# Kernel optimization log

Hardware: AMD Instinct MI355X
Metric: run time of the kernel (lower is better)

Reference implementation:

```python
import jax, jax.numpy as jnp
import numpy as np

N_NODES = 50000
N_EDGES = 800000
IN_CH = 256
OUT_CH = 128
HID = 2 * OUT_CH  # 256
LN_EPS = 1e-5


def _add_self_loops(edge_index, n):
    loop = jnp.arange(n, dtype=edge_index.dtype)
    src = jnp.concatenate([edge_index[0], loop])
    dst = jnp.concatenate([edge_index[1], loop])
    return src, dst


def _gcn_norm(src, dst, n):
    # PyG GCNConv norm: deg over source index, symmetric normalization
    ones = jnp.ones(src.shape[0], dtype=jnp.float32)
    deg = jax.ops.segment_sum(ones, src, num_segments=n)
    dinv = jnp.where(deg > 0, deg ** -0.5, 0.0)
    return dinv[src] * dinv[dst]  # [E+N]


def _gcn_conv(x, src, dst, norm, w, b, gamma=None, beta=None):
    h = x @ w                              # [N, out]
    msgs = norm[:, None] * h[src]          # gather + scale, [E+N, out]
    out = jax.ops.segment_sum(msgs, dst, num_segments=x.shape[0])
    if gamma is not None:
        out = gamma * out + beta           # FiLM modulation (per-feature)
    return out + b


def _layernorm(x):
    mu = jnp.mean(x, axis=-1, keepdims=True)
    var = jnp.var(x, axis=-1, keepdims=True)
    return (x - mu) * jax.lax.rsqrt(var + LN_EPS)


def setup_inputs() -> dict:
    key = jax.random.key(0)
    ks = jax.random.split(key, 20)

    def g(k, shape, scale=0.05):
        return jax.random.normal(k, shape, dtype=jnp.float32) * scale

    x = jax.random.normal(ks[0], (N_NODES, IN_CH), dtype=jnp.float32)
    edge_index = jax.random.randint(ks[1], (2, N_EDGES), 0, N_NODES, dtype=jnp.int64)
    return {
        "x": x,
        "edge_index": edge_index,
        "conv1_w": g(ks[2], (IN_CH, HID)),
        "conv1_b": g(ks[3], (HID,)),
        "conv2_w": g(ks[4], (HID, OUT_CH)),
        "conv2_b": g(ks[5], (OUT_CH,)),
        "sig_conv_w": g(ks[6], (IN_CH, HID)),
        "sig_conv_b": g(ks[7], (HID,)),
        "fc1_w": g(ks[8], (HID, HID)),
        "fc1_b": g(ks[9], (HID,)),
        "fc2_w": g(ks[10], (HID, HID)),
        "fc2_b": g(ks[11], (HID,)),
        "fc3_w": g(ks[12], (OUT_CH, HID)),
        "fc3_b": g(ks[13], (OUT_CH,)),
        "fc4_w": g(ks[14], (OUT_CH, HID)),
        "fc4_b": g(ks[15], (OUT_CH,)),
    }


def reference(x, edge_index, conv1_w, conv1_b, conv2_w, conv2_b,
              sig_conv_w, sig_conv_b, fc1_w, fc1_b, fc2_w, fc2_b,
              fc3_w, fc3_b, fc4_w, fc4_b):
    n = x.shape[0]
    src, dst = _add_self_loops(edge_index, n)
    norm = _gcn_norm(src, dst, n)

    # --- GraphSignature (use_gcn_sig=True) ---
    s = jax.nn.relu(_gcn_conv(x, src, dst, norm, sig_conv_w, sig_conv_b))
    s = s.sum(0)  # [HID]
    gamma1 = jnp.tanh(s @ fc1_w.T + fc1_b)  # [HID]
    beta1 = jnp.tanh(s @ fc2_w.T + fc2_b)   # [HID]
    gamma2 = jnp.tanh(s @ fc3_w.T + fc3_b)  # [OUT]
    beta2 = jnp.tanh(s @ fc4_w.T + fc4_b)   # [OUT]

    # inner_loop=True: signature outputs are detached
    gamma1, beta1, gamma2, beta2 = map(jax.lax.stop_gradient,
                                       (gamma1, beta1, gamma2, beta2))

    # --- Encoder (GAE) ---
    h = jax.nn.relu(_gcn_conv(x, src, dst, norm, conv1_w, conv1_b,
                              gamma=gamma1, beta=beta1))
    h = _layernorm(h)
    out = _gcn_conv(h, src, dst, norm, conv2_w, conv2_b,
                    gamma=gamma2, beta=beta2)
    out = _layernorm(out)
    return out
```

## Files before the change

### kernel.cpp

```cpp
#include <hip/hip_runtime.h>

typedef _Float16 f16;
typedef f16 f16x8 __attribute__((ext_vector_type(8)));
typedef float f32x4 __attribute__((ext_vector_type(4)));
typedef unsigned short u16;
typedef unsigned int u32;

#define IN_CH  256
#define HID    256
#define OUT_CH 128
#define LN_EPS 1e-5f
#define NSLOT  32
#define NR     8
#define NC     32
#define RS     6272
#define HT     512


__global__ __launch_bounds__(HT) void k_hist(const int* __restrict__ ei, int nE, int nN,
                                             int* __restrict__ hP,
                                             const float* __restrict__ x, f16* __restrict__ xh,
                                             int nelem, int nCast,
                                             const float* __restrict__ sigw,
                                             const float* __restrict__ c1w,
                                             const float* __restrict__ c2w,
                                             f16* __restrict__ Wt1, f16* __restrict__ Wt2) {
    int bid = blockIdx.x;
    if (bid < NR * NC) {
        __shared__ int h[RS];
        int r = bid & (NR - 1), c = bid >> 3;
        int rsz = (nN + NR - 1) / NR;
        int r0 = r * rsz;
        int sz = nN - r0; if (sz > rsz) sz = rsz;
        for (int i = threadIdx.x; i < sz; i += HT) h[i] = 0;
        __syncthreads();
        int nT = nE + nN;
        int chunk = (nT + NC - 1) / NC;
        int e0 = c * chunk, e1 = e0 + chunk; if (e1 > nT) e1 = nT;
        for (int eb = e0 + (int)threadIdx.x; eb < e1; eb += HT * 4) {
            int ss[4], dd[4];
            #pragma unroll
            for (int u = 0; u < 4; u++) {
                int e = eb + u * HT;
                ss[u] = -1; dd[u] = -1;
                if (e < e1) {
                    if (e < nE) { ss[u] = ei[e]; dd[u] = ei[nE + e]; }
                    else { ss[u] = e - nE; dd[u] = e - nE; }
                }
            }
            #pragma unroll
            for (int u = 0; u < 4; u++) {
                if ((unsigned)(ss[u] - r0) < (unsigned)sz) atomicAdd(&h[ss[u] - r0], 1);
                if ((unsigned)(dd[u] - r0) < (unsigned)sz) atomicAdd(&h[dd[u] - r0], 0x10000);
            }
        }
        __syncthreads();
        for (int i = threadIdx.x; i < sz; i += HT) hP[(size_t)c * nN + r0 + i] = h[i];
    } else if (bid < NR * NC + nCast) {
        int i = (bid - NR * NC) * 4096 + threadIdx.x * 8;
        if (i >= nelem) return;
        float4 a = *(const float4*)(x + i);
        float4 b = *(const float4*)(x + i + 4);
        f16x8 o = { (f16)a.x, (f16)a.y, (f16)a.z, (f16)a.w,
                    (f16)b.x, (f16)b.y, (f16)b.z, (f16)b.w };
        *(f16x8*)(xh + i) = o;
    } else {
        int i = (bid - NR * NC - nCast) * HT + threadIdx.x;
        if (i < 16384) {
            int ct = i >> 9;
            int rem = i & 511;
            int kx = rem >> 6;
            int lane = rem & 63;
            int q = lane >> 4, l = lane & 15;
            int n = (ct & 15) * 16 + l;
            int k0 = kx * 32 + q * 8;
            const float* src = (ct < 16) ? sigw : c1w;
            f16x8 o;
            #pragma unroll
            for (int j = 0; j < 8; j++) o[j] = (f16)src[(size_t)(k0 + j) * 256 + n];
            *(f16x8*)(Wt1 + (size_t)i * 8) = o;
        } else if (i < 20480) {
            int h2 = i - 16384;
            int ct = h2 >> 9;
            int rem = h2 & 511;
            int kx = rem >> 6;
            int lane = rem & 63;
            int q = lane >> 4, l = lane & 15;
            int n = ct * 16 + l;
            int k0 = kx * 32 + q * 8;
            f16x8 o;
            #pragma unroll
            for (int j = 0; j < 8; j++) o[j] = (f16)c2w[(size_t)(k0 + j) * 128 + n];
            *(f16x8*)(Wt2 + (size_t)h2 * 8) = o;
        }
    }
}


__global__ __launch_bounds__(256) void k_alloc(const int* __restrict__ hP,
                                               int* __restrict__ rowstart,
                                               int* __restrict__ chunkbase,
                                               int* __restrict__ cnt_tot,
                                               float* __restrict__ dinv,
                                               int* __restrict__ ctr, int nN) {
    int i = blockIdx.x * 256 + threadIdx.x;
    int lane = threadIdx.x & 63;
    int cnt = 0, dg = 0;
    if (i < nN) {
        for (int c = 0; c < NC; c++) {
            unsigned pk = (unsigned)hP[(size_t)c * nN + i];
            cnt += (int)(pk >> 16);
            dg  += (int)(pk & 0xffffu);
        }
    }
    int p = cnt;
    #pragma unroll
    for (int off = 1; off < 64; off <<= 1) {
        int v = __shfl_up(p, off, 64);
        if (lane >= off) p += v;
    }
    int tot = __shfl(p, 63, 64);
    int base = 0;
    if (lane == 0) base = atomicAdd(ctr, tot);
    base = __shfl(base, 0, 64);
    if (i < nN) {
        int nb = base + p - cnt;
        rowstart[i] = nb;
        cnt_tot[i] = cnt;
        dinv[i] = rsqrtf((float)dg);
        int run = nb;
        for (int c = 0; c < NC; c++) {
            chunkbase[(size_t)c * nN + i] = run;
            run += (int)((unsigned)hP[(size_t)c * nN + i] >> 16);
        }
    }
}


__global__ __launch_bounds__(HT) void k_fill(const int* __restrict__ ei, int nE, int nN,
                                             const int* __restrict__ chunkbase,
                                             u16* __restrict__ src_sorted) {
    __shared__ int pos_[RS];
    int r = blockIdx.x & (NR - 1), c = blockIdx.x >> 3;
    int rsz = (nN + NR - 1) / NR;
    int r0 = r * rsz;
    int sz = nN - r0; if (sz > rsz) sz = rsz;
    for (int i = threadIdx.x; i < sz; i += HT)
        pos_[i] = chunkbase[(size_t)c * nN + r0 + i];
    __syncthreads();
    int nT = nE + nN;
    int chunk = (nT + NC - 1) / NC;
    int e0 = c * chunk, e1 = e0 + chunk; if (e1 > nT) e1 = nT;
    for (int eb = e0 + (int)threadIdx.x; eb < e1; eb += HT * 4) {
        int ss[4], dd[4];
        #pragma unroll
        for (int u = 0; u < 4; u++) {
            int e = eb + u * HT;
            ss[u] = -1; dd[u] = -1;
            if (e < e1) {
                if (e < nE) { ss[u] = ei[e]; dd[u] = ei[nE + e]; }
                else { ss[u] = e - nE; dd[u] = e - nE; }
            }
        }
        #pragma unroll
        for (int u = 0; u < 4; u++) {
            int l = dd[u] - r0;
            if ((unsigned)l < (unsigned)sz) {
                int pos = atomicAdd(&pos_[l], 1);
                src_sorted[pos] = (u16)ss[u];
            }
        }
    }
}


__global__ __launch_bounds__(256) void k_aggX(const f16* __restrict__ xh,
                                              const int* __restrict__ rowstart,
                                              const int* __restrict__ counts,
                                              const u16* __restrict__ srcs,
                                              const float* __restrict__ dinv,
                                              f16* __restrict__ AX, int nN) {
    int wv = threadIdx.x >> 6;
    int lane = threadIdx.x & 63;
    int node = blockIdx.x * 4 + wv;
    if (node >= nN) return;
    int h = lane >> 5, sub = lane & 31;
    int beg = rowstart[node];
    int cnt = counts[node];
    float acc0[8] = {}, acc1[8] = {};
    for (int base = 0; base < cnt; base += 64) {
        int el = base + lane;
        int sv = 0; float dv = 0.f;
        if (el < cnt) { sv = srcs[beg + el]; dv = dinv[sv]; }
        int rem = cnt - base; if (rem > 64) rem = 64;
        int e = 0;
        for (; e + 16 <= rem; e += 16) {
            int s_[8]; float n_[8];
            #pragma unroll
            for (int u = 0; u < 8; u++) {
                int ii = e + u * 2 + h;
                s_[u] = __shfl(sv, ii, 64);
                n_[u] = __shfl(dv, ii, 64);
            }
            f16x8 v_[8];
            #pragma unroll
            for (int u = 0; u < 8; u++)
                v_[u] = *(const f16x8*)(xh + (size_t)s_[u] * 256 + sub * 8);
            #pragma unroll
            for (int u = 0; u < 8; u++)
                #pragma unroll
                for (int j = 0; j < 8; j++) {
                    float* a = (u & 1) ? acc1 : acc0;
                    a[j] = fmaf(n_[u], (float)v_[u][j], a[j]);
                }
        }
        for (; e < rem; e += 8) {
            int i0 = e + h, i1 = e + 2 + h, i2 = e + 4 + h, i3 = e + 6 + h;
            int sa = __shfl(sv, i0, 64), sb = __shfl(sv, i1, 64);
            int sc = __shfl(sv, i2, 64), sd = __shfl(sv, i3, 64);
            float na = __shfl(dv, i0, 64), nb = __shfl(dv, i1, 64);
            float nc = __shfl(dv, i2, 64), nd = __shfl(dv, i3, 64);
            if (i0 >= rem) na = 0.f;
            if (i1 >= rem) nb = 0.f;
            if (i2 >= rem) nc = 0.f;
            if (i3 >= rem) nd = 0.f;
            f16x8 va = *(const f16x8*)(xh + (size_t)sa * 256 + sub * 8);
            f16x8 vb = *(const f16x8*)(xh + (size_t)sb * 256 + sub * 8);
            f16x8 vc = *(const f16x8*)(xh + (size_t)sc * 256 + sub * 8);
            f16x8 vd = *(const f16x8*)(xh + (size_t)sd * 256 + sub * 8);
            #pragma unroll
            for (int j = 0; j < 8; j++) {
                acc0[j] = fmaf(na, (float)va[j], acc0[j]);
                acc1[j] = fmaf(nb, (float)vb[j], acc1[j]);
                acc0[j] = fmaf(nc, (float)vc[j], acc0[j]);
                acc1[j] = fmaf(nd, (float)vd[j], acc1[j]);
            }
        }
    }
    float dn = dinv[node];
    #pragma unroll
    for (int j = 0; j < 8; j++) {
        acc0[j] += acc1[j];
        acc0[j] += __shfl_xor(acc0[j], 32, 64);
    }
    if (lane < 32) {
        f16x8 o;
        #pragma unroll
        for (int j = 0; j < 8; j++) o[j] = (f16)(acc0[j] * dn);
        *(f16x8*)(AX + (size_t)node * 256 + sub * 8) = o;
    }
}


__global__ __launch_bounds__(256) void k_gemm_sig(const f16* __restrict__ AX,
                                                  const f16* __restrict__ Wt,
                                                  const float* __restrict__ sigb,
                                                  float* __restrict__ sig_part, int M) {
    __shared__ f16 axs[32][256];
    __shared__ f16 tile[32][264];
    f16* axl = &axs[0][0];
    int t = threadIdx.x;
    int w = t >> 6, lane = t & 63, quad = lane >> 4, l16 = lane & 15;
    int m0 = blockIdx.x * 32;
    {
        int tr = t >> 5;
        int c  = t & 31;
        #pragma unroll
        for (int p = 0; p < 4; p++) {
            int row = p * 8 + tr;
            int grow = m0 + row; if (grow >= M) grow = M - 1;
            *(f16x8*)(axl + row * 256 + ((c ^ tr) << 3)) =
                *(const f16x8*)(AX + (size_t)grow * 256 + c * 8);
        }
    }
    __syncthreads();
    int cb = w * 64;
    int sw = l16 & 7;
    f32x4 acc[2][4] = {};
    for (int kx = 0; kx < 8; kx++) {
        int c0 = (kx * 4 + quad) ^ sw;
        f16x8 a[2];
        a[0] = *(const f16x8*)(axl + l16 * 256 + (c0 << 3));
        a[1] = *(const f16x8*)(axl + (16 + l16) * 256 + (c0 << 3));
        #pragma unroll
        for (int ns = 0; ns < 4; ns++) {
            int ct = w * 4 + ns;
            f16x8 b = *(const f16x8*)(Wt + ((size_t)((ct * 8 + kx) * 64 + lane) << 3));
            acc[0][ns] = __builtin_amdgcn_mfma_f32_16x16x32_f16(a[0], b, acc[0][ns], 0, 0, 0);
            acc[1][ns] = __builtin_amdgcn_mfma_f32_16x16x32_f16(a[1], b, acc[1][ns], 0, 0, 0);
        }
    }
    #pragma unroll
    for (int ms = 0; ms < 2; ms++)
        #pragma unroll
        for (int ns = 0; ns < 4; ns++)
            #pragma unroll
            for (int r = 0; r < 4; r++) {
                int mr = ms * 16 + quad * 4 + r;
                int c = cb + ns * 16 + l16;
                float v = fmaxf(acc[ms][ns][r] + sigb[c], 0.f);
                if (m0 + mr >= M) v = 0.f;
                tile[mr][c] = (f16)v;
            }
    __syncthreads();
    float s = 0.f;
    #pragma unroll 8
    for (int r = 0; r < 32; r++) s += (float)tile[r][t];
    atomicAdd(&sig_part[(blockIdx.x & (NSLOT - 1)) * 256 + t], s);
}


__global__ __launch_bounds__(256) void k_fc(const float* __restrict__ sig_part,
                                            const float* __restrict__ f1w, const float* __restrict__ f1b,
                                            const float* __restrict__ f2w, const float* __restrict__ f2b,
                                            const float* __restrict__ f3w, const float* __restrict__ f3b,
                                            const float* __restrict__ f4w, const float* __restrict__ f4b,
                                            const float* __restrict__ c1b, const float* __restrict__ c2b,
                                            float* __restrict__ g1, float* __restrict__ bc1,
                                            float* __restrict__ g2, float* __restrict__ bc2) {
    __shared__ float ss[256];
    int t = threadIdx.x;
    float s = 0.f;
    for (int k = 0; k < NSLOT; k++) s += sig_part[k * 256 + t];
    ss[t] = s;
    __syncthreads();
    int wv = t >> 6, lane = t & 63;
    float s0 = ss[lane], s1 = ss[lane + 64], s2v = ss[lane + 128], s3 = ss[lane + 192];
    #pragma unroll
    for (int rr = 0; rr < 16; rr++) {
        int row = blockIdx.x * 64 + wv * 16 + rr;
        const float* w; const float* bb; const float* ex; float* dst; int r;
        if (row < 256)      { w = f1w; bb = f1b; dst = g1;  ex = 0;   r = row; }
        else if (row < 512) { w = f2w; bb = f2b; dst = bc1; ex = c1b; r = row - 256; }
        else if (row < 640) { w = f3w; bb = f3b; dst = g2;  ex = 0;   r = row - 512; }
        else                { w = f4w; bb = f4b; dst = bc2; ex = c2b; r = row - 640; }
        const float* wr = w + (size_t)r * 256;
        float a = wr[lane] * s0;
        a = fmaf(wr[lane + 64], s1, a);
        a = fmaf(wr[lane + 128], s2v, a);
        a = fmaf(wr[lane + 192], s3, a);
        #pragma unroll
        for (int off = 1; off < 64; off <<= 1) a += __shfl_xor(a, off, 64);
        if (lane == 0) dst[r] = tanhf(a + bb[r]) + (ex ? ex[r] : 0.f);
    }
}


__global__ __launch_bounds__(256) void k_c1f(const f16* __restrict__ AX,
                                             const f16* __restrict__ Wt,
                                             const f16* __restrict__ Wt2,
                                             const float* __restrict__ g1,
                                             const float* __restrict__ bc1,
                                             const float* __restrict__ dinv,
                                             f16* __restrict__ HW, int M) {
    __shared__ f16 axs[32][256];
    __shared__ f16 ht[32][264];
    __shared__ float ps[32][5], ps2[32][5];
    __shared__ float mu_[32], rr_[32], sdinv[32];
    f16* axl = &axs[0][0];
    int t = threadIdx.x;
    int w = t >> 6, lane = t & 63, quad = lane >> 4, l16 = lane & 15;
    int m0 = blockIdx.x * 32;
    int cb = w * 64;
    {
        int tr = t >> 5;
        int c  = t & 31;
        #pragma unroll
        for (int p = 0; p < 4; p++) {
            int row = p * 8 + tr;
            int grow = m0 + row; if (grow >= M) grow = M - 1;
            *(f16x8*)(axl + row * 256 + ((c ^ tr) << 3)) =
                *(const f16x8*)(AX + (size_t)grow * 256 + c * 8);
        }
    }
    __syncthreads();
    int sw = l16 & 7;
    f32x4 acc[2][4] = {};
    for (int kx = 0; kx < 8; kx++) {
        int c0 = (kx * 4 + quad) ^ sw;
        f16x8 a[2];
        a[0] = *(const f16x8*)(axl + l16 * 256 + (c0 << 3));
        a[1] = *(const f16x8*)(axl + (16 + l16) * 256 + (c0 << 3));
        #pragma unroll
        for (int ns = 0; ns < 4; ns++) {
            int ct = w * 4 + ns;
            f16x8 b = *(const f16x8*)(Wt + ((size_t)((ct * 8 + kx) * 64 + lane) << 3));
            acc[0][ns] = __builtin_amdgcn_mfma_f32_16x16x32_f16(a[0], b, acc[0][ns], 0, 0, 0);
            acc[1][ns] = __builtin_amdgcn_mfma_f32_16x16x32_f16(a[1], b, acc[1][ns], 0, 0, 0);
        }
    }

    float rs[2][4] = {{0.f,0.f,0.f,0.f},{0.f,0.f,0.f,0.f}};
    float rs2[2][4] = {{0.f,0.f,0.f,0.f},{0.f,0.f,0.f,0.f}};
    #pragma unroll
    for (int ns = 0; ns < 4; ns++) {
        int c = cb + ns * 16 + l16;
        float gv = g1[c], bv = bc1[c];
        #pragma unroll
        for (int ms = 0; ms < 2; ms++)
            #pragma unroll
            for (int r = 0; r < 4; r++) {
                float v = fmaxf(fmaf(gv, acc[ms][ns][r], bv), 0.f);
                acc[ms][ns][r] = v;
                rs[ms][r] += v;
                rs2[ms][r] = fmaf(v, v, rs2[ms][r]);
            }
    }
    #pragma unroll
    for (int off = 1; off < 16; off <<= 1)
        #pragma unroll
        for (int ms = 0; ms < 2; ms++)
            #pragma unroll
            for (int r = 0; r < 4; r++) {
                rs[ms][r]  += __shfl_xor(rs[ms][r], off, 64);
                rs2[ms][r] += __shfl_xor(rs2[ms][r], off, 64);
            }
    if (l16 == 0) {
        #pragma unroll
        for (int ms = 0; ms < 2; ms++)
            #pragma unroll
            for (int r = 0; r < 4; r++) {
                int mr = ms * 16 + quad * 4 + r;
                ps[mr][w] = rs[ms][r];
                ps2[mr][w] = rs2[ms][r];
            }
    }
    __syncthreads();
    if (t < 32) {
        float S = ps[t][0] + ps[t][1] + ps[t][2] + ps[t][3];
        float S2 = ps2[t][0] + ps2[t][1] + ps2[t][2] + ps2[t][3];
        float mu = S * (1.f / 256.f);
        mu_[t] = mu;
        rr_[t] = rsqrtf(S2 * (1.f / 256.f) - mu * mu + LN_EPS);
        int m = m0 + t;
        sdinv[t] = (m < M) ? dinv[m] : 0.f;
    }
    __syncthreads();
    #pragma unroll
    for (int ms = 0; ms < 2; ms++)
        #pragma unroll
        for (int r = 0; r < 4; r++) {
            int mr = ms * 16 + quad * 4 + r;
            float mu = mu_[mr], rr = rr_[mr];
            #pragma unroll
            for (int ns = 0; ns < 4; ns++)
                ht[mr][cb + ns * 16 + l16] = (f16)((acc[ms][ns][r] - mu) * rr);
        }
    __syncthreads();
    int cb2 = w * 32;
    f32x4 acc2[2][2] = {};
    for (int kx = 0; kx < 8; kx++) {
        int ka = kx * 32 + quad * 8;
        f16x8 a[2];
        #pragma unroll
        for (int ms = 0; ms < 2; ms++)
            a[ms] = *(const f16x8*)(&ht[ms * 16 + l16][ka]);
        #pragma unroll
        for (int ns = 0; ns < 2; ns++) {
            int ct = w * 2 + ns;
            f16x8 b = *(const f16x8*)(Wt2 + ((size_t)((ct * 8 + kx) * 64 + lane) << 3));
            acc2[0][ns] = __builtin_amdgcn_mfma_f32_16x16x32_f16(a[0], b, acc2[0][ns], 0, 0, 0);
            acc2[1][ns] = __builtin_amdgcn_mfma_f32_16x16x32_f16(a[1], b, acc2[1][ns], 0, 0, 0);
        }
    }
    #pragma unroll
    for (int ms = 0; ms < 2; ms++)
        #pragma unroll
        for (int ns = 0; ns < 2; ns++)
            #pragma unroll
            for (int r = 0; r < 4; r++) {
                int mr = ms * 16 + quad * 4 + r;
                int m = m0 + mr;
                if (m < M) HW[(size_t)m * 128 + cb2 + ns * 16 + l16] = (f16)(acc2[ms][ns][r] * sdinv[mr]);
            }
}


__global__ __launch_bounds__(256) void k_agg2(const f16* __restrict__ HW,
                                              const int* __restrict__ rowstart,
                                              const int* __restrict__ counts,
                                              const u16* __restrict__ srcs,
                                              const float* __restrict__ dinv,
                                              const float* __restrict__ g2,
                                              const float* __restrict__ bc2,
                                              float* __restrict__ out, int nN) {
    int wv = threadIdx.x >> 6;
    int lane = threadIdx.x & 63;
    int node = blockIdx.x * 4 + wv;
    if (node >= nN) return;
    int q = lane >> 4, sub = lane & 15;
    int beg = rowstart[node];
    int cnt = counts[node];
    float acc0[8] = {}, acc1[8] = {};
    for (int base = 0; base < cnt; base += 64) {
        int el = base + lane;
        int sv = 0; float dv = 0.f;
        if (el < cnt) { sv = srcs[beg + el]; dv = 1.f; }
        int rem = cnt - base; if (rem > 64) rem = 64;
        int e = 0;
        for (; e + 16 <= rem; e += 16) {
            int s_[4]; float n_[4];
            #pragma unroll
            for (int u = 0; u < 4; u++) {
                int ii = e + u * 4 + q;
                s_[u] = __shfl(sv, ii, 64);
                n_[u] = __shfl(dv, ii, 64);
            }
            f16x8 v_[4];
            #pragma unroll
            for (int u = 0; u < 4; u++)
                v_[u] = *(const f16x8*)(HW + (size_t)s_[u] * 128 + sub * 8);
            #pragma unroll
            for (int u = 0; u < 4; u++)
                #pragma unroll
                for (int j = 0; j < 8; j++) {
                    float* a = (u & 1) ? acc1 : acc0;
                    a[j] = fmaf(n_[u], (float)v_[u][j], a[j]);
                }
        }
        for (; e < rem; e += 8) {
            int i0 = e + q, i1 = e + 4 + q;
            int sa = __shfl(sv, i0, 64), sb = __shfl(sv, i1, 64);
            float na = __shfl(dv, i0, 64), nb = __shfl(dv, i1, 64);
            if (i0 >= rem) na = 0.f;
            if (i1 >= rem) nb = 0.f;
            f16x8 va = *(const f16x8*)(HW + (size_t)sa * 128 + sub * 8);
            f16x8 vb = *(const f16x8*)(HW + (size_t)sb * 128 + sub * 8);
            #pragma unroll
            for (int j = 0; j < 8; j++) {
                acc0[j] = fmaf(na, (float)va[j], acc0[j]);
                acc1[j] = fmaf(nb, (float)vb[j], acc1[j]);
            }
        }
    }
    float dn = dinv[node];
    #pragma unroll
    for (int j = 0; j < 8; j++) {
        acc0[j] += acc1[j];
        acc0[j] += __shfl_xor(acc0[j], 16, 64);
        acc0[j] += __shfl_xor(acc0[j], 32, 64);
    }
    int ch = sub * 8;
    float vfin[8];
    float s = 0.f, s2 = 0.f;
    #pragma unroll
    for (int j = 0; j < 8; j++) {
        float v = fmaf(g2[ch + j], acc0[j] * dn, bc2[ch + j]);
        vfin[j] = v;
        s += v; s2 = fmaf(v, v, s2);
    }
    #pragma unroll
    for (int off = 1; off < 16; off <<= 1) {
        s += __shfl_xor(s, off, 64);
        s2 += __shfl_xor(s2, off, 64);
    }
    float mu = s * (1.f / 128.f);
    float rr = rsqrtf(s2 * (1.f / 128.f) - mu * mu + LN_EPS);
    if (q == 0) {
        float4 o0 = { (vfin[0] - mu) * rr, (vfin[1] - mu) * rr,
                      (vfin[2] - mu) * rr, (vfin[3] - mu) * rr };
        float4 o1 = { (vfin[4] - mu) * rr, (vfin[5] - mu) * rr,
                      (vfin[6] - mu) * rr, (vfin[7] - mu) * rr };
        float* dst = out + (size_t)node * 128 + ch;
        *(float4*)dst = o0;
        *(float4*)(dst + 4) = o1;
    }
}


extern "C" void kernel_launch(void* const* d_in, const int* in_sizes, int n_in,
                              void* d_out, int out_size, void* d_ws, size_t ws_size,
                              hipStream_t stream) {
    const float* x    = (const float*)d_in[0];
    const int*   ei   = (const int*)d_in[1];
    const float* c1w  = (const float*)d_in[2];
    const float* c1b  = (const float*)d_in[3];
    const float* c2w  = (const float*)d_in[4];
    const float* c2b  = (const float*)d_in[5];
    const float* sigw = (const float*)d_in[6];
    const float* sigb = (const float*)d_in[7];
    const float* f1w  = (const float*)d_in[8];
    const float* f1b  = (const float*)d_in[9];
    const float* f2w  = (const float*)d_in[10];
    const float* f2b  = (const float*)d_in[11];
    const float* f3w  = (const float*)d_in[12];
    const float* f3b  = (const float*)d_in[13];
    const float* f4w  = (const float*)d_in[14];
    const float* f4b  = (const float*)d_in[15];
    float* out = (float*)d_out;

    int nN = in_sizes[0] / IN_CH;
    int nE = in_sizes[1] / 2;
    int nT = nE + nN;

    char* base = (char*)d_ws;
    size_t off = 0;
    auto alloc = [&](size_t bytes) { size_t o = off; off += (bytes + 255) & ~(size_t)255; return o; };

    size_t o_spart  = alloc((size_t)NSLOT * 256 * 4);
    size_t o_ctr    = alloc(256);
    size_t zero_bytes = off;
    size_t o_hP     = alloc((size_t)NC * nN * 4);
    size_t o_cbase  = alloc((size_t)NC * nN * 4);
    size_t o_g1     = alloc(256 * 4);
    size_t o_b1     = alloc(256 * 4);
    size_t o_g2     = alloc(128 * 4);
    size_t o_b2     = alloc(128 * 4);
    size_t o_rowst  = alloc((size_t)nN * 4);
    size_t o_cntt   = alloc((size_t)nN * 4);
    size_t o_dinv   = alloc((size_t)nN * 4);
    size_t o_src    = alloc((size_t)nT * 2);
    size_t o_wt1    = alloc(512 * 256 * 2);
    size_t o_wt2    = alloc(128 * 256 * 2);
    size_t o_xh     = alloc((size_t)nN * 256 * 2);
    size_t o_AX     = alloc((size_t)nN * 256 * 2);
    size_t o_HW     = alloc((size_t)nN * 128 * 2);

    float* spart  = (float*)(base + o_spart);
    int*   ctr    = (int*)(base + o_ctr);
    int*   hP     = (int*)(base + o_hP);
    int*   cbase  = (int*)(base + o_cbase);
    float* g1     = (float*)(base + o_g1);
    float* bc1    = (float*)(base + o_b1);
    float* g2     = (float*)(base + o_g2);
    float* bc2    = (float*)(base + o_b2);
    int*   rowst  = (int*)(base + o_rowst);
    int*   cntt   = (int*)(base + o_cntt);
    float* dinv   = (float*)(base + o_dinv);
    u16*   srcs   = (u16*)(base + o_src);
    f16*   Wt1    = (f16*)(base + o_wt1);
    f16*   Wt2    = (f16*)(base + o_wt2);
    f16*   xh     = (f16*)(base + o_xh);
    f16*   AX     = (f16*)(base + o_AX);
    f16*   HW     = (f16*)(base + o_HW);

    hipMemsetAsync(base, 0, zero_bytes, stream);

    int nCast = (nN * IN_CH + 4095) / 4096;
    int nPrep = (20480 + HT - 1) / HT;
    k_hist<<<NR * NC + nCast + nPrep, HT, 0, stream>>>(ei, nE, nN, hP,
                                                       x, xh, nN * IN_CH, nCast,
                                                       sigw, c1w, c2w, Wt1, Wt2);

    k_alloc<<<(nN + 255) / 256, 256, 0, stream>>>(hP, rowst, cbase, cntt, dinv, ctr, nN);

    k_fill<<<NR * NC, HT, 0, stream>>>(ei, nE, nN, cbase, srcs);

    int nb4 = (nN + 3) / 4;
    int mg = (nN + 31) / 32;
    k_aggX<<<nb4, 256, 0, stream>>>(xh, rowst, cntt, srcs, dinv, AX, nN);
    k_gemm_sig<<<mg, 256, 0, stream>>>(AX, Wt1, sigb, spart, nN);
    k_fc<<<12, 256, 0, stream>>>(spart, f1w, f1b, f2w, f2b, f3w, f3b, f4w, f4b,
                                 c1b, c2b, g1, bc1, g2, bc2);
    k_c1f<<<mg, 256, 0, stream>>>(AX, Wt1 + 256 * 256, Wt2, g1, bc1, dinv, HW, nN);
    k_agg2<<<nb4, 256, 0, stream>>>(HW, rowst, cntt, srcs, dinv, g2, bc2, out, nN);
}
```

Before: 310.3 us.

## Prescale fp16 features by dinv in fill kernel, drop per-edge dinv gathers

```diff
diff --git a/kernel.cpp b/kernel.cpp
--- a/kernel.cpp
+++ b/kernel.cpp
@@ -139,37 +139,50 @@
 
 __global__ __launch_bounds__(HT) void k_fill(const int* __restrict__ ei, int nE, int nN,
                                              const int* __restrict__ chunkbase,
-                                             u16* __restrict__ src_sorted) {
-    __shared__ int pos_[RS];
-    int r = blockIdx.x & (NR - 1), c = blockIdx.x >> 3;
-    int rsz = (nN + NR - 1) / NR;
-    int r0 = r * rsz;
-    int sz = nN - r0; if (sz > rsz) sz = rsz;
-    for (int i = threadIdx.x; i < sz; i += HT)
-        pos_[i] = chunkbase[(size_t)c * nN + r0 + i];
-    __syncthreads();
-    int nT = nE + nN;
-    int chunk = (nT + NC - 1) / NC;
-    int e0 = c * chunk, e1 = e0 + chunk; if (e1 > nT) e1 = nT;
-    for (int eb = e0 + (int)threadIdx.x; eb < e1; eb += HT * 4) {
-        int ss[4], dd[4];
-        #pragma unroll
-        for (int u = 0; u < 4; u++) {
-            int e = eb + u * HT;
-            ss[u] = -1; dd[u] = -1;
-            if (e < e1) {
-                if (e < nE) { ss[u] = ei[e]; dd[u] = ei[nE + e]; }
-                else { ss[u] = e - nE; dd[u] = e - nE; }
-            }
-        }
-        #pragma unroll
-        for (int u = 0; u < 4; u++) {
-            int l = dd[u] - r0;
-            if ((unsigned)l < (unsigned)sz) {
-                int pos = atomicAdd(&pos_[l], 1);
-                src_sorted[pos] = (u16)ss[u];
-            }
-        }
+                                             u16* __restrict__ src_sorted,
+                                             const float* __restrict__ dinv,
+                                             f16* __restrict__ xh, int nelem) {
+    int bid = blockIdx.x;
+    if (bid < NR * NC) {
+        __shared__ int pos_[RS];
+        int r = bid & (NR - 1), c = bid >> 3;
+        int rsz = (nN + NR - 1) / NR;
+        int r0 = r * rsz;
+        int sz = nN - r0; if (sz > rsz) sz = rsz;
+        for (int i = threadIdx.x; i < sz; i += HT)
+            pos_[i] = chunkbase[(size_t)c * nN + r0 + i];
+        __syncthreads();
+        int nT = nE + nN;
+        int chunk = (nT + NC - 1) / NC;
+        int e0 = c * chunk, e1 = e0 + chunk; if (e1 > nT) e1 = nT;
+        for (int eb = e0 + (int)threadIdx.x; eb < e1; eb += HT * 4) {
+            int ss[4], dd[4];
+            #pragma unroll
+            for (int u = 0; u < 4; u++) {
+                int e = eb + u * HT;
+                ss[u] = -1; dd[u] = -1;
+                if (e < e1) {
+                    if (e < nE) { ss[u] = ei[e]; dd[u] = ei[nE + e]; }
+                    else { ss[u] = e - nE; dd[u] = e - nE; }
+                }
+            }
+            #pragma unroll
+            for (int u = 0; u < 4; u++) {
+                int l = dd[u] - r0;
+                if ((unsigned)l < (unsigned)sz) {
+                    int pos = atomicAdd(&pos_[l], 1);
+                    src_sorted[pos] = (u16)ss[u];
+                }
+            }
+        }
+    } else {
+        int i = (bid - NR * NC) * 4096 + threadIdx.x * 8;
+        if (i >= nelem) return;
+        float dn = dinv[i >> 8];
+        f16x8 v = *(const f16x8*)(xh + i);
+        #pragma unroll
+        for (int j = 0; j < 8; j++) v[j] = (f16)((float)v[j] * dn);
+        *(f16x8*)(xh + i) = v;
     }
 }
 
@@ -190,18 +203,14 @@
     float acc0[8] = {}, acc1[8] = {};
     for (int base = 0; base < cnt; base += 64) {
         int el = base + lane;
-        int sv = 0; float dv = 0.f;
-        if (el < cnt) { sv = srcs[beg + el]; dv = dinv[sv]; }
+        int sv = (el < cnt) ? (int)srcs[beg + el] : 0;
         int rem = cnt - base; if (rem > 64) rem = 64;
         int e = 0;
         for (; e + 16 <= rem; e += 16) {
-            int s_[8]; float n_[8];
-            #pragma unroll
-            for (int u = 0; u < 8; u++) {
-                int ii = e + u * 2 + h;
-                s_[u] = __shfl(sv, ii, 64);
-                n_[u] = __shfl(dv, ii, 64);
-            }
+            int s_[8];
+            #pragma unroll
+            for (int u = 0; u < 8; u++)
+                s_[u] = __shfl(sv, e + u * 2 + h, 64);
             f16x8 v_[8];
             #pragma unroll
             for (int u = 0; u < 8; u++)
@@ -211,19 +220,17 @@
                 #pragma unroll
                 for (int j = 0; j < 8; j++) {
                     float* a = (u & 1) ? acc1 : acc0;
-                    a[j] = fmaf(n_[u], (float)v_[u][j], a[j]);
+                    a[j] += (float)v_[u][j];
                 }
         }
         for (; e < rem; e += 8) {
             int i0 = e + h, i1 = e + 2 + h, i2 = e + 4 + h, i3 = e + 6 + h;
             int sa = __shfl(sv, i0, 64), sb = __shfl(sv, i1, 64);
             int sc = __shfl(sv, i2, 64), sd = __shfl(sv, i3, 64);
-            float na = __shfl(dv, i0, 64), nb = __shfl(dv, i1, 64);
-            float nc = __shfl(dv, i2, 64), nd = __shfl(dv, i3, 64);
-            if (i0 >= rem) na = 0.f;
-            if (i1 >= rem) nb = 0.f;
-            if (i2 >= rem) nc = 0.f;
-            if (i3 >= rem) nd = 0.f;
+            float na = (i0 < rem) ? 1.f : 0.f;
+            float nb = (i1 < rem) ? 1.f : 0.f;
+            float nc = (i2 < rem) ? 1.f : 0.f;
+            float nd = (i3 < rem) ? 1.f : 0.f;
             f16x8 va = *(const f16x8*)(xh + (size_t)sa * 256 + sub * 8);
             f16x8 vb = *(const f16x8*)(xh + (size_t)sb * 256 + sub * 8);
             f16x8 vc = *(const f16x8*)(xh + (size_t)sc * 256 + sub * 8);
@@ -494,36 +501,31 @@
     float acc0[8] = {}, acc1[8] = {};
     for (int base = 0; base < cnt; base += 64) {
         int el = base + lane;
-        int sv = 0; float dv = 0.f;
-        if (el < cnt) { sv = srcs[beg + el]; dv = 1.f; }
+        int sv = (el < cnt) ? (int)srcs[beg + el] : 0;
         int rem = cnt - base; if (rem > 64) rem = 64;
         int e = 0;
-        for (; e + 16 <= rem; e += 16) {
-            int s_[4]; float n_[4];
-            #pragma unroll
-            for (int u = 0; u < 4; u++) {
-                int ii = e + u * 4 + q;
-                s_[u] = __shfl(sv, ii, 64);
-                n_[u] = __shfl(dv, ii, 64);
-            }
-            f16x8 v_[4];
-            #pragma unroll
-            for (int u = 0; u < 4; u++)
+        for (; e + 32 <= rem; e += 32) {
+            int s_[8];
+            #pragma unroll
+            for (int u = 0; u < 8; u++)
+                s_[u] = __shfl(sv, e + u * 4 + q, 64);
+            f16x8 v_[8];
+            #pragma unroll
+            for (int u = 0; u < 8; u++)
                 v_[u] = *(const f16x8*)(HW + (size_t)s_[u] * 128 + sub * 8);
             #pragma unroll
-            for (int u = 0; u < 4; u++)
+            for (int u = 0; u < 8; u++)
                 #pragma unroll
                 for (int j = 0; j < 8; j++) {
                     float* a = (u & 1) ? acc1 : acc0;
-                    a[j] = fmaf(n_[u], (float)v_[u][j], a[j]);
+                    a[j] += (float)v_[u][j];
                 }
         }
         for (; e < rem; e += 8) {
             int i0 = e + q, i1 = e + 4 + q;
             int sa = __shfl(sv, i0, 64), sb = __shfl(sv, i1, 64);
-            float na = __shfl(dv, i0, 64), nb = __shfl(dv, i1, 64);
-            if (i0 >= rem) na = 0.f;
-            if (i1 >= rem) nb = 0.f;
+            float na = (i0 < rem) ? 1.f : 0.f;
+            float nb = (i1 < rem) ? 1.f : 0.f;
             f16x8 va = *(const f16x8*)(HW + (size_t)sa * 128 + sub * 8);
             f16x8 vb = *(const f16x8*)(HW + (size_t)sb * 128 + sub * 8);
             #pragma unroll
@@ -644,7 +646,8 @@
 
     k_alloc<<<(nN + 255) / 256, 256, 0, stream>>>(hP, rowst, cbase, cntt, dinv, ctr, nN);
 
-    k_fill<<<NR * NC, HT, 0, stream>>>(ei, nE, nN, cbase, srcs);
+    int nScale = (nN * IN_CH + 4095) / 4096;
+    k_fill<<<NR * NC + nScale, HT, 0, stream>>>(ei, nE, nN, cbase, srcs, dinv, xh, nN * IN_CH);
 
     int nb4 = (nN + 3) / 4;
     int mg = (nN + 31) / 32;
```

Measured after the change: 326.5 us. +5.2%, slower.

## Fuse X aggregation into signature GEMM and batch 32 nodes per block in agg2

Applied to the files above, without the earlier changes.

```diff
diff --git a/kernel.cpp b/kernel.cpp
--- a/kernel.cpp
+++ b/kernel.cpp
@@ -174,106 +174,95 @@
 }
 
 
-__global__ __launch_bounds__(256) void k_aggX(const f16* __restrict__ xh,
-                                              const int* __restrict__ rowstart,
-                                              const int* __restrict__ counts,
-                                              const u16* __restrict__ srcs,
-                                              const float* __restrict__ dinv,
-                                              f16* __restrict__ AX, int nN) {
-    int wv = threadIdx.x >> 6;
-    int lane = threadIdx.x & 63;
-    int node = blockIdx.x * 4 + wv;
-    if (node >= nN) return;
-    int h = lane >> 5, sub = lane & 31;
-    int beg = rowstart[node];
-    int cnt = counts[node];
-    float acc0[8] = {}, acc1[8] = {};
-    for (int base = 0; base < cnt; base += 64) {
-        int el = base + lane;
-        int sv = 0; float dv = 0.f;
-        if (el < cnt) { sv = srcs[beg + el]; dv = dinv[sv]; }
-        int rem = cnt - base; if (rem > 64) rem = 64;
-        int e = 0;
-        for (; e + 16 <= rem; e += 16) {
-            int s_[8]; float n_[8];
-            #pragma unroll
-            for (int u = 0; u < 8; u++) {
-                int ii = e + u * 2 + h;
-                s_[u] = __shfl(sv, ii, 64);
-                n_[u] = __shfl(dv, ii, 64);
-            }
-            f16x8 v_[8];
-            #pragma unroll
-            for (int u = 0; u < 8; u++)
-                v_[u] = *(const f16x8*)(xh + (size_t)s_[u] * 256 + sub * 8);
-            #pragma unroll
-            for (int u = 0; u < 8; u++)
-                #pragma unroll
-                for (int j = 0; j < 8; j++) {
-                    float* a = (u & 1) ? acc1 : acc0;
-                    a[j] = fmaf(n_[u], (float)v_[u][j], a[j]);
-                }
-        }
-        for (; e < rem; e += 8) {
-            int i0 = e + h, i1 = e + 2 + h, i2 = e + 4 + h, i3 = e + 6 + h;
-            int sa = __shfl(sv, i0, 64), sb = __shfl(sv, i1, 64);
-            int sc = __shfl(sv, i2, 64), sd = __shfl(sv, i3, 64);
-            float na = __shfl(dv, i0, 64), nb = __shfl(dv, i1, 64);
-            float nc = __shfl(dv, i2, 64), nd = __shfl(dv, i3, 64);
-            if (i0 >= rem) na = 0.f;
-            if (i1 >= rem) nb = 0.f;
-            if (i2 >= rem) nc = 0.f;
-            if (i3 >= rem) nd = 0.f;
-            f16x8 va = *(const f16x8*)(xh + (size_t)sa * 256 + sub * 8);
-            f16x8 vb = *(const f16x8*)(xh + (size_t)sb * 256 + sub * 8);
-            f16x8 vc = *(const f16x8*)(xh + (size_t)sc * 256 + sub * 8);
-            f16x8 vd = *(const f16x8*)(xh + (size_t)sd * 256 + sub * 8);
-            #pragma unroll
-            for (int j = 0; j < 8; j++) {
-                acc0[j] = fmaf(na, (float)va[j], acc0[j]);
-                acc1[j] = fmaf(nb, (float)vb[j], acc1[j]);
-                acc0[j] = fmaf(nc, (float)vc[j], acc0[j]);
-                acc1[j] = fmaf(nd, (float)vd[j], acc1[j]);
-            }
-        }
-    }
-    float dn = dinv[node];
-    #pragma unroll
-    for (int j = 0; j < 8; j++) {
-        acc0[j] += acc1[j];
-        acc0[j] += __shfl_xor(acc0[j], 32, 64);
-    }
-    if (lane < 32) {
-        f16x8 o;
-        #pragma unroll
-        for (int j = 0; j < 8; j++) o[j] = (f16)(acc0[j] * dn);
-        *(f16x8*)(AX + (size_t)node * 256 + sub * 8) = o;
-    }
-}
-
-
-__global__ __launch_bounds__(256) void k_gemm_sig(const f16* __restrict__ AX,
-                                                  const f16* __restrict__ Wt,
-                                                  const float* __restrict__ sigb,
-                                                  float* __restrict__ sig_part, int M) {
+__global__ __launch_bounds__(256) void k_aggsig(const f16* __restrict__ xh,
+                                                const int* __restrict__ rowstart,
+                                                const int* __restrict__ counts,
+                                                const u16* __restrict__ srcs,
+                                                const float* __restrict__ dinv,
+                                                const f16* __restrict__ Wt,
+                                                const float* __restrict__ sigb,
+                                                f16* __restrict__ AX,
+                                                float* __restrict__ sig_part, int M) {
     __shared__ f16 axs[32][256];
     __shared__ f16 tile[32][264];
     f16* axl = &axs[0][0];
     int t = threadIdx.x;
-    int w = t >> 6, lane = t & 63, quad = lane >> 4, l16 = lane & 15;
+    int wv = t >> 6, lane = t & 63;
+    int h = lane >> 5, sub = lane & 31;
     int m0 = blockIdx.x * 32;
-    {
-        int tr = t >> 5;
-        int c  = t & 31;
-        #pragma unroll
-        for (int p = 0; p < 4; p++) {
-            int row = p * 8 + tr;
-            int grow = m0 + row; if (grow >= M) grow = M - 1;
-            *(f16x8*)(axl + row * 256 + ((c ^ tr) << 3)) =
-                *(const f16x8*)(AX + (size_t)grow * 256 + c * 8);
-        }
-    }
-    __syncthreads();
+
+    for (int k = 0; k < 8; k++) {
+        int row = wv * 8 + k;
+        int node = m0 + row;
+        int beg = 0, cnt = 0;
+        if (node < M) { beg = rowstart[node]; cnt = counts[node]; }
+        float acc0[8] = {}, acc1[8] = {};
+        for (int base = 0; base < cnt; base += 64) {
+            int el = base + lane;
+            int sv = 0; float dv = 0.f;
+            if (el < cnt) { sv = srcs[beg + el]; dv = dinv[sv]; }
+            int rem = cnt - base; if (rem > 64) rem = 64;
+            int e = 0;
+            for (; e + 16 <= rem; e += 16) {
+                int s_[8]; float n_[8];
+                #pragma unroll
+                for (int u = 0; u < 8; u++) {
+                    int ii = e + u * 2 + h;
+                    s_[u] = __shfl(sv, ii, 64);
+                    n_[u] = __shfl(dv, ii, 64);
+                }
+                f16x8 v_[8];
+                #pragma unroll
+                for (int u = 0; u < 8; u++)
+                    v_[u] = *(const f16x8*)(xh + (size_t)s_[u] * 256 + sub * 8);
+                #pragma unroll
+                for (int u = 0; u < 8; u++)
+                    #pragma unroll
+                    for (int j = 0; j < 8; j++) {
+                        float* a = (u & 1) ? acc1 : acc0;
+                        a[j] = fmaf(n_[u], (float)v_[u][j], a[j]);
+                    }
+            }
+            for (; e < rem; e += 8) {
+                int i0 = e + h, i1 = e + 2 + h, i2 = e + 4 + h, i3 = e + 6 + h;
+                int sa = __shfl(sv, i0, 64), sb = __shfl(sv, i1, 64);
+                int sc = __shfl(sv, i2, 64), sd = __shfl(sv, i3, 64);
+                float na = __shfl(dv, i0, 64), nb = __shfl(dv, i1, 64);
+                float nc = __shfl(dv, i2, 64), nd = __shfl(dv, i3, 64);
+                if (i0 >= rem) na = 0.f;
+                if (i1 >= rem) nb = 0.f;
+                if (i2 >= rem) nc = 0.f;
+                if (i3 >= rem) nd = 0.f;
+                f16x8 va = *(const f16x8*)(xh + (size_t)sa * 256 + sub * 8);
+                f16x8 vb = *(const f16x8*)(xh + (size_t)sb * 256 + sub * 8);
+                f16x8 vc = *(const f16x8*)(xh + (size_t)sc * 256 + sub * 8);
+                f16x8 vd = *(const f16x8*)(xh + (size_t)sd * 256 + sub * 8);
+                #pragma unroll
+                for (int j = 0; j < 8; j++) {
+                    acc0[j] = fmaf(na, (float)va[j], acc0[j]);
+                    acc1[j] = fmaf(nb, (float)vb[j], acc1[j]);
+                    acc0[j] = fmaf(nc, (float)vc[j], acc0[j]);
+                    acc1[j] = fmaf(nd, (float)vd[j], acc1[j]);
+                }
+            }
+        }
+        float dn = (node < M) ? dinv[node] : 0.f;
+        #pragma unroll
+        for (int j = 0; j < 8; j++) {
+            acc0[j] += acc1[j];
+            acc0[j] += __shfl_xor(acc0[j], 32, 64);
+        }
+        if (lane < 32) {
+            f16x8 o;
+            #pragma unroll
+            for (int j = 0; j < 8; j++) o[j] = (f16)(acc0[j] * dn);
+            if (node < M) *(f16x8*)(AX + (size_t)node * 256 + sub * 8) = o;
+            *(f16x8*)(axl + row * 256 + ((sub ^ (row & 7)) << 3)) = o;
+        }
+    }
+    __syncthreads();
+
+    int w = wv, quad = lane >> 4, l16 = lane & 15;
     int cb = w * 64;
     int sw = l16 & 7;
     f32x4 acc[2][4] = {};
@@ -486,84 +475,82 @@
                                               float* __restrict__ out, int nN) {
     int wv = threadIdx.x >> 6;
     int lane = threadIdx.x & 63;
-    int node = blockIdx.x * 4 + wv;
-    if (node >= nN) return;
     int q = lane >> 4, sub = lane & 15;
-    int beg = rowstart[node];
-    int cnt = counts[node];
-    float acc0[8] = {}, acc1[8] = {};
-    for (int base = 0; base < cnt; base += 64) {
-        int el = base + lane;
-        int sv = 0; float dv = 0.f;
-        if (el < cnt) { sv = srcs[beg + el]; dv = 1.f; }
-        int rem = cnt - base; if (rem > 64) rem = 64;
-        int e = 0;
-        for (; e + 16 <= rem; e += 16) {
-            int s_[4]; float n_[4];
-            #pragma unroll
-            for (int u = 0; u < 4; u++) {
-                int ii = e + u * 4 + q;
-                s_[u] = __shfl(sv, ii, 64);
-                n_[u] = __shfl(dv, ii, 64);
-            }
-            f16x8 v_[4];
-            #pragma unroll
-            for (int u = 0; u < 4; u++)
-                v_[u] = *(const f16x8*)(HW + (size_t)s_[u] * 128 + sub * 8);
-            #pragma unroll
-            for (int u = 0; u < 4; u++)
+    int m0 = blockIdx.x * 32;
+    for (int k = 0; k < 8; k++) {
+        int node = m0 + wv * 8 + k;
+        if (node >= nN) continue;
+        int beg = rowstart[node];
+        int cnt = counts[node];
+        float acc0[8] = {}, acc1[8] = {};
+        for (int base = 0; base < cnt; base += 64) {
+            int el = base + lane;
+            int sv = (el < cnt) ? (int)srcs[beg + el] : 0;
+            int rem = cnt - base; if (rem > 64) rem = 64;
+            int e = 0;
+            for (; e + 32 <= rem; e += 32) {
+                int s_[8];
+                #pragma unroll
+                for (int u = 0; u < 8; u++)
+                    s_[u] = __shfl(sv, e + u * 4 + q, 64);
+                f16x8 v_[8];
+                #pragma unroll
+                for (int u = 0; u < 8; u++)
+                    v_[u] = *(const f16x8*)(HW + (size_t)s_[u] * 128 + sub * 8);
+                #pragma unroll
+                for (int u = 0; u < 8; u++)
+                    #pragma unroll
+                    for (int j = 0; j < 8; j++) {
+                        float* a = (u & 1) ? acc1 : acc0;
+                        a[j] += (float)v_[u][j];
+                    }
+            }
+            for (; e < rem; e += 8) {
+                int i0 = e + q, i1 = e + 4 + q;
+                int sa = __shfl(sv, i0, 64), sb = __shfl(sv, i1, 64);
+                float na = (i0 < rem) ? 1.f : 0.f;
+                float nb = (i1 < rem) ? 1.f : 0.f;
+                f16x8 va = *(const f16x8*)(HW + (size_t)sa * 128 + sub * 8);
+                f16x8 vb = *(const f16x8*)(HW + (size_t)sb * 128 + sub * 8);
                 #pragma unroll
                 for (int j = 0; j < 8; j++) {
-                    float* a = (u & 1) ? acc1 : acc0;
-                    a[j] = fmaf(n_[u], (float)v_[u][j], a[j]);
+                    acc0[j] = fmaf(na, (float)va[j], acc0[j]);
+                    acc1[j] = fmaf(nb, (float)vb[j], acc1[j]);
                 }
-        }
-        for (; e < rem; e += 8) {
-            int i0 = e + q, i1 = e + 4 + q;
-            int sa = __shfl(sv, i0, 64), sb = __shfl(sv, i1, 64);
-            float na = __shfl(dv, i0, 64), nb = __shfl(dv, i1, 64);
-            if (i0 >= rem) na = 0.f;
-            if (i1 >= rem) nb = 0.f;
-            f16x8 va = *(const f16x8*)(HW + (size_t)sa * 128 + sub * 8);
-            f16x8 vb = *(const f16x8*)(HW + (size_t)sb * 128 + sub * 8);
-            #pragma unroll
-            for (int j = 0; j < 8; j++) {
-                acc0[j] = fmaf(na, (float)va[j], acc0[j]);
-                acc1[j] = fmaf(nb, (float)vb[j], acc1[j]);
-            }
-        }
-    }
-    float dn = dinv[node];
-    #pragma unroll
-    for (int j = 0; j < 8; j++) {
-        acc0[j] += acc1[j];
-        acc0[j] += __shfl_xor(acc0[j], 16, 64);
-        acc0[j] += __shfl_xor(acc0[j], 32, 64);
-    }
-    int ch = sub * 8;
-    float vfin[8];
-    float s = 0.f, s2 = 0.f;
-    #pragma unroll
-    for (int j = 0; j < 8; j++) {
-        float v = fmaf(g2[ch + j], acc0[j] * dn, bc2[ch + j]);
-        vfin[j] = v;
-        s += v; s2 = fmaf(v, v, s2);
-    }
-    #pragma unroll
-    for (int off = 1; off < 16; off <<= 1) {
-        s += __shfl_xor(s, off, 64);
-        s2 += __shfl_xor(s2, off, 64);
-    }
-    float mu = s * (1.f / 128.f);
-    float rr = rsqrtf(s2 * (1.f / 128.f) - mu * mu + LN_EPS);
-    if (q == 0) {
-        float4 o0 = { (vfin[0] - mu) * rr, (vfin[1] - mu) * rr,
-                      (vfin[2] - mu) * rr, (vfin[3] - mu) * rr };
-        float4 o1 = { (vfin[4] - mu) * rr, (vfin[5] - mu) * rr,
-                      (vfin[6] - mu) * rr, (vfin[7] - mu) * rr };
-        float* dst = out + (size_t)node * 128 + ch;
-        *(float4*)dst = o0;
-        *(float4*)(dst + 4) = o1;
+            }
+        }
+        float dn = dinv[node];
+        #pragma unroll
+        for (int j = 0; j < 8; j++) {
+            acc0[j] += acc1[j];
+            acc0[j] += __shfl_xor(acc0[j], 16, 64);
+            acc0[j] += __shfl_xor(acc0[j], 32, 64);
+        }
+        int ch = sub * 8;
+        float vfin[8];
+        float s = 0.f, s2 = 0.f;
+        #pragma unroll
+        for (int j = 0; j < 8; j++) {
+            float v = fmaf(g2[ch + j], acc0[j] * dn, bc2[ch + j]);
+            vfin[j] = v;
+            s += v; s2 = fmaf(v, v, s2);
+        }
+        #pragma unroll
+        for (int off = 1; off < 16; off <<= 1) {
+            s += __shfl_xor(s, off, 64);
+            s2 += __shfl_xor(s2, off, 64);
+        }
+        float mu = s * (1.f / 128.f);
+        float rr = rsqrtf(s2 * (1.f / 128.f) - mu * mu + LN_EPS);
+        if (q == 0) {
+            float4 o0 = { (vfin[0] - mu) * rr, (vfin[1] - mu) * rr,
+                          (vfin[2] - mu) * rr, (vfin[3] - mu) * rr };
+            float4 o1 = { (vfin[4] - mu) * rr, (vfin[5] - mu) * rr,
+                          (vfin[6] - mu) * rr, (vfin[7] - mu) * rr };
+            float* dst = out + (size_t)node * 128 + ch;
+            *(float4*)dst = o0;
+            *(float4*)(dst + 4) = o1;
+        }
     }
 }
 
@@ -646,12 +633,10 @@
 
     k_fill<<<NR * NC, HT, 0, stream>>>(ei, nE, nN, cbase, srcs);
 
-    int nb4 = (nN + 3) / 4;
     int mg = (nN + 31) / 32;
-    k_aggX<<<nb4, 256, 0, stream>>>(xh, rowst, cntt, srcs, dinv, AX, nN);
-    k_gemm_sig<<<mg, 256, 0, stream>>>(AX, Wt1, sigb, spart, nN);
+    k_aggsig<<<mg, 256, 0, stream>>>(xh, rowst, cntt, srcs, dinv, Wt1, sigb, AX, spart, nN);
     k_fc<<<12, 256, 0, stream>>>(spart, f1w, f1b, f2w, f2b, f3w, f3b, f4w, f4b,
                                  c1b, c2b, g1, bc1, g2, bc2);
     k_c1f<<<mg, 256, 0, stream>>>(AX, Wt1 + 256 * 256, Wt2, g1, bc1, dinv, HW, nN);
-    k_agg2<<<nb4, 256, 0, stream>>>(HW, rowst, cntt, srcs, dinv, g2, bc2, out, nN);
-}
+    k_agg2<<<mg, 256, 0, stream>>>(HW, rowst, cntt, srcs, dinv, g2, bc2, out, nN);
+}
```

New measurement: 334.9 us. 1.08x slower.
